# Kernel optimization log

Measured on AMD Instinct MI355X. Metric: run time of the kernel, lower is better.

## Reference

```python
import jax, jax.numpy as jnp
import numpy as np

B, W, N, DIM, GAMMA = 32, 16, 256, 256, 4
WH = 16  # sqrt(N)
V = DIM // GAMMA
TABLE = (2 * WH - 1) * (2 * WH - 1)  # 961


def _make_rel_index(wh: int) -> np.ndarray:
    coords = np.stack(np.meshgrid(np.arange(wh), np.arange(wh), indexing='ij'))  # (2, wh, wh)
    flat = coords.reshape(2, -1)                         # (2, wh*wh)
    rel = flat[:, :, None] - flat[:, None, :]            # (2, n, n)
    rel = rel.transpose(1, 2, 0).copy()                  # (n, n, 2)
    rel[:, :, 0] += wh - 1
    rel[:, :, 1] += wh - 1
    rel[:, :, 0] *= 2 * wh - 1
    return rel.sum(-1).astype(np.int32)                  # (n, n)


def setup_inputs() -> dict:
    key = jax.random.key(0)
    k1, k2, k3 = jax.random.split(key, 3)
    x = jax.random.normal(k1, (B, W, N, DIM), dtype=jnp.float32)
    bias_table = jax.random.normal(k2, (TABLE, W * GAMMA), dtype=jnp.float32) * 0.02
    token_bias = jax.random.normal(k3, (W * GAMMA, N, 1), dtype=jnp.float32) * 0.02
    rel_index = jnp.asarray(_make_rel_index(WH))
    return {"x": x, "bias_table": bias_table, "token_bias": token_bias, "rel_index": rel_index}


def reference(x, bias_table, token_bias, rel_index):
    b, w, n, d = x.shape
    gamma = GAMMA
    v = d // gamma
    # gather: (n, n, w*gamma) -> permute to (w*gamma, n, n)
    rpb = bias_table[rel_index.reshape(-1)].reshape(n, n, w * gamma)
    rpb = jnp.transpose(rpb, (2, 0, 1))                  # ((s w), n, n) with s outer
    # rearrange '(s b) m n -> b m n s'
    win_weight = jnp.transpose(rpb.reshape(gamma, w, n, n), (1, 2, 3, 0))  # (w, m, n, s)
    # rearrange 'b w n (v s) -> b w n v s'
    xs = x.reshape(b, w, n, v, gamma)
    out = jnp.einsum('wmns,bwnvs->bwmvs', win_weight, xs)
    # rearrange '(w s) m v -> w m v s'
    bias = jnp.transpose(token_bias.reshape(w, gamma, n, 1), (0, 2, 3, 1))  # (w, m, 1, s)
    out = out + bias[None]
    return out.reshape(b, w, n, d)
```

## Files before the change

### kernel.cpp

```cpp
#include <hip/hip_runtime.h>
#include <stdint.h>


typedef __attribute__((ext_vector_type(8))) short bf16x8;
typedef __attribute__((ext_vector_type(4))) float f32x4;
typedef __attribute__((ext_vector_type(8))) unsigned short u16x8;

__device__ __forceinline__ unsigned short f2bf(float f) {
    union { float f; unsigned u; } v; v.f = f;
    unsigned u = v.u;
    u += 0x7FFFu + ((u >> 16) & 1u);
    return (unsigned short)(u >> 16);
}
__device__ __forceinline__ float bf2f(unsigned short h) {
    union { unsigned u; float f; } v; v.u = ((unsigned)h) << 16;
    return v.f;
}
__device__ __forceinline__ int expInRange(unsigned short w16) {
    int e = (w16 >> 7) & 0xFF;
    return (e >= 100 && e <= 140) ? 1 : 0;
}

#define GLL16(gp, lp) __builtin_amdgcn_global_load_lds( \
    (const __attribute__((address_space(1))) void*)(gp), \
    (__attribute__((address_space(3))) void*)(lp), 16, 0, 0)

__global__ __launch_bounds__(256) void k_gather(
    const void* __restrict__ bt_raw,
    const int*  __restrict__ rel_index,
    const void* __restrict__ x_raw,
    unsigned short* __restrict__ Ab)
{
    __shared__ unsigned short Lt[64 * 72];

    const unsigned short* xw = (const unsigned short*)x_raw;
    int t = threadIdx.x;
    int pred = expInRange(xw[t * 2]) & expInRange(xw[t * 2 + 1]);
    int cnt = __syncthreads_count(pred);
    bool isF32 = (cnt < 150);

    const int cellbase = blockIdx.x << 6;
    const int c = t >> 2;
    const int p = t & 3;
    const int row = rel_index[cellbase + c];

    unsigned short vals[16];
    if (isF32) {
        const float* bt = (const float*)bt_raw + (row << 6) + (p << 4);
        float4 v0 = *(const float4*)(bt);
        float4 v1 = *(const float4*)(bt + 4);
        float4 v2 = *(const float4*)(bt + 8);
        float4 v3 = *(const float4*)(bt + 12);
        float vf[16] = {v0.x,v0.y,v0.z,v0.w, v1.x,v1.y,v1.z,v1.w,
                        v2.x,v2.y,v2.z,v2.w, v3.x,v3.y,v3.z,v3.w};
#pragma unroll
        for (int k = 0; k < 16; k++) vals[k] = f2bf(vf[k]);
    } else {
        const unsigned short* bt = (const unsigned short*)bt_raw + (row << 6) + (p << 4);
        u16x8 a0 = *(const u16x8*)(bt);
        u16x8 a1 = *(const u16x8*)(bt + 8);
#pragma unroll
        for (int k = 0; k < 8; k++) { vals[k] = a0[k]; vals[8 + k] = a1[k]; }
    }
#pragma unroll
    for (int k = 0; k < 16; k++)
        Lt[(((k << 2) + p) * 72) + c] = vals[k];
    __syncthreads();

    const int plane = t >> 2;
    const int cg = (t & 3) << 4;
    u16x8 o0 = *(const u16x8*)(Lt + plane * 72 + cg);
    u16x8 o1 = *(const u16x8*)(Lt + plane * 72 + cg + 8);
    unsigned short* dst = Ab + (plane << 16) + cellbase + cg;
    *(u16x8*)dst = o0;
    *(u16x8*)(dst + 8) = o1;
}

__global__ __launch_bounds__(512, 4) void k_main(
    const void* __restrict__ x_raw,
    const unsigned short* __restrict__ Ab,
    const void* __restrict__ tb_raw,
    void* __restrict__ out_raw)
{
    __shared__ unsigned short lds[16384];

    const int tid  = threadIdx.x;
    const unsigned short* xw = (const unsigned short*)x_raw;
    int pred = expInRange(xw[tid]);
    int cnt = __syncthreads_count(pred);
    const bool isF32 = (cnt < 400);

    const int lane = tid & 63;
    const int wave = tid >> 6;
    const int bx = blockIdx.x;
    const int swz = ((bx & 7) << 8) | (bx >> 3);
    const int mt = swz & 3;
    const int b  = (swz >> 2) & 31;
    const int w  = swz >> 7;
    const int m0 = mt << 6;

    const int sw   = wave & 3;
    const int vh   = wave >> 2;
    const int vvb  = vh << 5;
    const int col  = lane & 15;
    const int quad = lane >> 4;

    const int amRow   = (tid >> 2) & 63;
    const int aswslot = (tid & 3) ^ ((amRow >> 1) & 3);
    const unsigned short* Ag0 = Ab + (((w << 2) + (tid >> 8)) << 16)
                                   + ((m0 + amRow) << 8) + (aswslot << 3);
    const unsigned short* Ag1 = Ag0 + (2 << 16);
    const int aswz = (col >> 1) & 3;
    const int ar = (sw << 11) + (col << 5) + ((quad ^ aswz) << 3);

    const int d0   = (tid & 127) << 1;
    const int ngrp = tid >> 7;
    const int xgoff = (((b << 4) + w) << 16) + (ngrp << 11) + d0;
    const float*          Xgf = (const float*)x_raw + xgoff;
    const unsigned short* Xgh = (const unsigned short*)x_raw + xgoff;
    const int vvx   = d0 >> 2;
    const int xslot = ((ngrp ^ ((vvx >> 1) & 3)) << 3);
    unsigned short* xw0p = lds + 8192 + ((d0 & 3) << 11) + (vvx << 5) + xslot;
    unsigned short* xw1p = xw0p + 2048;

    const int xr0 = 8192 + (sw << 11) + ((vvb + col) << 5) + ((quad ^ aswz) << 3);
    const int xr1 = xr0 + 512;

    f32x4 acc[4][2];
#pragma unroll
    for (int mi = 0; mi < 4; mi++) {
        acc[mi][0] = (f32x4){0.f, 0.f, 0.f, 0.f};
        acc[mi][1] = (f32x4){0.f, 0.f, 0.f, 0.f};
    }

    for (int nc = 0; nc < 8; ++nc) {
        GLL16(Ag0 + (nc << 5), lds + (wave << 9));
        GLL16(Ag1 + (nc << 5), lds + 4096 + (wave << 9));

        u16x8 o0, o1;
        if (isF32) {
            float2 v[8];
#pragma unroll
            for (int j = 0; j < 8; j++)
                v[j] = *(const float2*)(Xgf + (nc << 13) + (j << 8));
#pragma unroll
            for (int j = 0; j < 8; j++) { o0[j] = f2bf(v[j].x); o1[j] = f2bf(v[j].y); }
        } else {
            unsigned int v[8];
#pragma unroll
            for (int j = 0; j < 8; j++)
                v[j] = *(const unsigned int*)(Xgh + (nc << 13) + (j << 8));
#pragma unroll
            for (int j = 0; j < 8; j++) { o0[j] = (unsigned short)(v[j] & 0xFFFFu);
                                          o1[j] = (unsigned short)(v[j] >> 16); }
        }
        *(u16x8*)xw0p = o0;
        *(u16x8*)xw1p = o1;
        __syncthreads();

        bf16x8 bfr0 = *(const bf16x8*)(lds + xr0);
        bf16x8 bfr1 = *(const bf16x8*)(lds + xr1);
#pragma unroll
        for (int mi = 0; mi < 4; mi++) {
            bf16x8 afr = *(const bf16x8*)(lds + ar + (mi << 9));
            acc[mi][0] = __builtin_amdgcn_mfma_f32_16x16x32_bf16(afr, bfr0, acc[mi][0], 0, 0, 0);
            acc[mi][1] = __builtin_amdgcn_mfma_f32_16x16x32_bf16(afr, bfr1, acc[mi][1], 0, 0, 0);
        }
        __syncthreads();
    }

    const int tboff = (((w << 2) + sw) << 8) + m0;
    const int ooff  = (((b << 4) + w) << 16) + (m0 << 8) + sw;
    if (isF32) {
        const float* tb = (const float*)tb_raw + tboff;
        float* ob = (float*)out_raw + ooff;
#pragma unroll
        for (int mi = 0; mi < 4; mi++) {
#pragma unroll
            for (int r = 0; r < 4; r++) {
                int m = (mi << 4) + (quad << 2) + r;
                float bias = tb[m];
#pragma unroll
                for (int vi = 0; vi < 2; vi++) {
                    int vv = vvb + (vi << 4) + col;
                    ob[(m << 8) + (vv << 2)] = acc[mi][vi][r] + bias;
                }
            }
        }
    } else {
        const unsigned short* tb = (const unsigned short*)tb_raw + tboff;
        unsigned short* ob = (unsigned short*)out_raw + ooff;
#pragma unroll
        for (int mi = 0; mi < 4; mi++) {
#pragma unroll
            for (int r = 0; r < 4; r++) {
                int m = (mi << 4) + (quad << 2) + r;
                float bias = bf2f(tb[m]);
#pragma unroll
                for (int vi = 0; vi < 2; vi++) {
                    int vv = vvb + (vi << 4) + col;
                    ob[(m << 8) + (vv << 2)] = f2bf(acc[mi][vi][r] + bias);
                }
            }
        }
    }
}

__global__ __launch_bounds__(512, 4) void k_main_fused(
    const void* __restrict__ x_raw,
    const void* __restrict__ bt_raw,
    const int*  __restrict__ rel_index,
    const void* __restrict__ tb_raw,
    void* __restrict__ out_raw)
{
    __shared__ unsigned short lds[16384 + 8192];

    const int tid  = threadIdx.x;
    const unsigned short* xw = (const unsigned short*)x_raw;
    int pred = expInRange(xw[tid]);
    int cnt = __syncthreads_count(pred);
    const bool isF32 = (cnt < 400);

    const int lane = tid & 63;
    const int wave = tid >> 6;
    const int bx = blockIdx.x;
    const int b  = bx & 31;
    const int mt = (bx >> 5) & 1;
    const int w  = bx >> 6;
    const int m0 = mt << 7;

    const int sw   = wave & 3;
    const int vh   = wave >> 2;
    const int vvb  = vh << 5;
    const int col  = lane & 15;
    const int quad = lane >> 4;

    const int a_row = tid >> 2;
    const int a_nn8 = (tid & 3) << 3;
    unsigned short* AsW = lds + (a_row << 5) + a_nn8;
    const int* rIp = rel_index + ((m0 + a_row) << 8) + a_nn8;

    const int x_nn = tid & 31;
    const int x_vg = tid >> 5;
    const int xoff = (((b << 4) + w) << 16) + (x_nn << 8) + (x_vg << 4);
    const float*          Xgf = (const float*)x_raw + xoff;
    const unsigned short* Xgh = (const unsigned short*)x_raw + xoff;
    unsigned short* XsW = lds + 16384 + x_nn;

    f32x4 acc[8][2];
#pragma unroll
    for (int mi = 0; mi < 8; mi++) {
        acc[mi][0] = (f32x4){0.f, 0.f, 0.f, 0.f};
        acc[mi][1] = (f32x4){0.f, 0.f, 0.f, 0.f};
    }

    const unsigned short* AsR = lds + (sw << 12) + (col << 5) + (quad << 3);
    const unsigned short* XsR = lds + 16384 + (sw << 11) + ((vvb + col) << 5) + (quad << 3);

    for (int nc = 0; nc < 8; nc++) {
        int4 r0 = *(const int4*)(rIp + (nc << 5));
        int4 r1 = *(const int4*)(rIp + (nc << 5) + 4);
        int ri[8] = {r0.x, r0.y, r0.z, r0.w, r1.x, r1.y, r1.z, r1.w};
#pragma unroll
        for (int it = 0; it < 4; it++) {
            u16x8 av;
            if (isF32) {
                const float* bt = (const float*)bt_raw;
#pragma unroll
                for (int j = 0; j < 8; j++)
                    av[j] = f2bf(bt[(ri[j] << 6) + (it << 4) + w]);
            } else {
                const unsigned short* bt = (const unsigned short*)bt_raw;
#pragma unroll
                for (int j = 0; j < 8; j++)
                    av[j] = bt[(ri[j] << 6) + (it << 4) + w];
            }
            *(u16x8*)(AsW + (it << 12)) = av;
        }

        if (isF32) {
            float4 v[4];
#pragma unroll
            for (int i = 0; i < 4; i++)
                v[i] = *(const float4*)(Xgf + (nc << 13) + (i << 2));
            const float* vf = (const float*)v;
#pragma unroll
            for (int j = 0; j < 16; j++) {
                int vv = (x_vg << 2) + (j >> 2);
                XsW[((j & 3) << 11) + (vv << 5)] = f2bf(vf[j]);
            }
        } else {
            u16x8 xv0 = *(const u16x8*)(Xgh + (nc << 13));
            u16x8 xv1 = *(const u16x8*)(Xgh + (nc << 13) + 8);
#pragma unroll
            for (int j = 0; j < 8; j++) {
                int vv = (x_vg << 2) + (j >> 2);
                XsW[((j & 3) << 11) + (vv << 5)] = xv0[j];
            }
#pragma unroll
            for (int j = 0; j < 8; j++) {
                int vv = (x_vg << 2) + 2 + (j >> 2);
                XsW[((j & 3) << 11) + (vv << 5)] = xv1[j];
            }
        }
        __syncthreads();

        bf16x8 bfr0 = *(const bf16x8*)(XsR);
        bf16x8 bfr1 = *(const bf16x8*)(XsR + 512);
#pragma unroll
        for (int mi = 0; mi < 8; mi++) {
            bf16x8 afr = *(const bf16x8*)(AsR + (mi << 9));
            acc[mi][0] = __builtin_amdgcn_mfma_f32_16x16x32_bf16(afr, bfr0, acc[mi][0], 0, 0, 0);
            acc[mi][1] = __builtin_amdgcn_mfma_f32_16x16x32_bf16(afr, bfr1, acc[mi][1], 0, 0, 0);
        }
        __syncthreads();
    }

    const int tboff = (((w << 2) + sw) << 8) + m0;
    const int ooff  = (((b << 4) + w) << 16) + (m0 << 8) + sw;
    if (isF32) {
        const float* tb = (const float*)tb_raw + tboff;
        float* ob = (float*)out_raw + ooff;
#pragma unroll
        for (int mi = 0; mi < 8; mi++) {
#pragma unroll
            for (int r = 0; r < 4; r++) {
                int m = (mi << 4) + (quad << 2) + r;
                float bias = tb[m];
#pragma unroll
                for (int vi = 0; vi < 2; vi++) {
                    int vv = vvb + (vi << 4) + col;
                    ob[(m << 8) + (vv << 2)] = acc[mi][vi][r] + bias;
                }
            }
        }
    } else {
        const unsigned short* tb = (const unsigned short*)tb_raw + tboff;
        unsigned short* ob = (unsigned short*)out_raw + ooff;
#pragma unroll
        for (int mi = 0; mi < 8; mi++) {
#pragma unroll
            for (int r = 0; r < 4; r++) {
                int m = (mi << 4) + (quad << 2) + r;
                float bias = bf2f(tb[m]);
#pragma unroll
                for (int vi = 0; vi < 2; vi++) {
                    int vv = vvb + (vi << 4) + col;
                    ob[(m << 8) + (vv << 2)] = f2bf(acc[mi][vi][r] + bias);
                }
            }
        }
    }
}

extern "C" void kernel_launch(void* const* d_in, const int* in_sizes, int n_in,
                              void* d_out, int out_size, void* d_ws, size_t ws_size,
                              hipStream_t stream) {
    const void* x          = d_in[0];
    const void* bias_table = d_in[1];
    const void* token_bias = d_in[2];
    const int*  rel_index  = (const int*)d_in[3];

    const size_t AB_BYTES = (size_t)64 * 256 * 256 * 2;
    if (ws_size >= AB_BYTES) {
        unsigned short* Ab = (unsigned short*)d_ws;
        hipLaunchKernelGGL(k_gather, dim3(1024), dim3(256), 0, stream,
                           bias_table, rel_index, x, Ab);
        hipLaunchKernelGGL(k_main, dim3(2048), dim3(512), 0, stream,
                           x, Ab, token_bias, d_out);
    } else {
        hipLaunchKernelGGL(k_main_fused, dim3(1024), dim3(512), 0, stream,
                           x, bias_table, rel_index, token_bias, d_out);
    }
}
```

Baseline: 307.0 us.

## Double the M tile per block and prefetch next X chunk into registers

Each block now computes 128 output rows instead of 64. The grid is halved, so each staged X tile is reused across twice as many MFMAs, which halves redundant X reads and conversions. The next n-chunk of X is also loaded into registers during the current chunk's compute, to hide global load latency. In exchange, LDS grows to 48KB, accumulator registers double, and fewer blocks mean lower occupancy and parallelism.

```diff
diff --git a/kernel.cpp b/kernel.cpp
--- a/kernel.cpp
+++ b/kernel.cpp
@@ -82,7 +82,7 @@
     const void* __restrict__ tb_raw,
     void* __restrict__ out_raw)
 {
-    __shared__ unsigned short lds[16384];
+    __shared__ unsigned short lds[24576];
 
     const int tid  = threadIdx.x;
     const unsigned short* xw = (const unsigned short*)x_raw;
@@ -93,11 +93,11 @@
     const int lane = tid & 63;
     const int wave = tid >> 6;
     const int bx = blockIdx.x;
-    const int swz = ((bx & 7) << 8) | (bx >> 3);
-    const int mt = swz & 3;
-    const int b  = (swz >> 2) & 31;
-    const int w  = swz >> 7;
-    const int m0 = mt << 6;
+    const int swz = ((bx & 7) << 7) | (bx >> 3);
+    const int mt = swz & 1;
+    const int b  = (swz >> 1) & 31;
+    const int w  = swz >> 6;
+    const int m0 = mt << 7;
 
     const int sw   = wave & 3;
     const int vh   = wave >> 2;
@@ -105,13 +105,11 @@
     const int col  = lane & 15;
     const int quad = lane >> 4;
 
-    const int amRow   = (tid >> 2) & 63;
+    const int amRow   = (tid >> 2) & 127;
     const int aswslot = (tid & 3) ^ ((amRow >> 1) & 3);
-    const unsigned short* Ag0 = Ab + (((w << 2) + (tid >> 8)) << 16)
-                                   + ((m0 + amRow) << 8) + (aswslot << 3);
-    const unsigned short* Ag1 = Ag0 + (2 << 16);
+    const unsigned short* AgB = Ab + ((m0 + amRow) << 8) + (aswslot << 3);
     const int aswz = (col >> 1) & 3;
-    const int ar = (sw << 11) + (col << 5) + ((quad ^ aswz) << 3);
+    const int ar = (sw << 12) + (col << 5) + ((quad ^ aswz) << 3);
 
     const int d0   = (tid & 127) << 1;
     const int ngrp = tid >> 7;
@@ -120,48 +118,65 @@
     const unsigned short* Xgh = (const unsigned short*)x_raw + xgoff;
     const int vvx   = d0 >> 2;
     const int xslot = ((ngrp ^ ((vvx >> 1) & 3)) << 3);
-    unsigned short* xw0p = lds + 8192 + ((d0 & 3) << 11) + (vvx << 5) + xslot;
+    unsigned short* xw0p = lds + 16384 + ((d0 & 3) << 11) + (vvx << 5) + xslot;
     unsigned short* xw1p = xw0p + 2048;
 
-    const int xr0 = 8192 + (sw << 11) + ((vvb + col) << 5) + ((quad ^ aswz) << 3);
+    const int xr0 = 16384 + (sw << 11) + ((vvb + col) << 5) + ((quad ^ aswz) << 3);
     const int xr1 = xr0 + 512;
 
-    f32x4 acc[4][2];
-#pragma unroll
-    for (int mi = 0; mi < 4; mi++) {
+    f32x4 acc[8][2];
+#pragma unroll
+    for (int mi = 0; mi < 8; mi++) {
         acc[mi][0] = (f32x4){0.f, 0.f, 0.f, 0.f};
         acc[mi][1] = (f32x4){0.f, 0.f, 0.f, 0.f};
     }
 
+    float2       xf[8];
+    unsigned int xu[8];
+    if (isF32) {
+#pragma unroll
+        for (int j = 0; j < 8; j++) xf[j] = *(const float2*)(Xgf + (j << 8));
+    } else {
+#pragma unroll
+        for (int j = 0; j < 8; j++) xu[j] = *(const unsigned int*)(Xgh + (j << 8));
+    }
+
+#pragma unroll
     for (int nc = 0; nc < 8; ++nc) {
-        GLL16(Ag0 + (nc << 5), lds + (wave << 9));
-        GLL16(Ag1 + (nc << 5), lds + 4096 + (wave << 9));
+#pragma unroll
+        for (int c = 0; c < 4; c++)
+            GLL16(AgB + (((w << 2) + c) << 16) + (nc << 5),
+                  lds + (c << 12) + (wave << 9));
 
         u16x8 o0, o1;
         if (isF32) {
-            float2 v[8];
-#pragma unroll
-            for (int j = 0; j < 8; j++)
-                v[j] = *(const float2*)(Xgf + (nc << 13) + (j << 8));
-#pragma unroll
-            for (int j = 0; j < 8; j++) { o0[j] = f2bf(v[j].x); o1[j] = f2bf(v[j].y); }
+#pragma unroll
+            for (int j = 0; j < 8; j++) { o0[j] = f2bf(xf[j].x); o1[j] = f2bf(xf[j].y); }
         } else {
-            unsigned int v[8];
-#pragma unroll
-            for (int j = 0; j < 8; j++)
-                v[j] = *(const unsigned int*)(Xgh + (nc << 13) + (j << 8));
-#pragma unroll
-            for (int j = 0; j < 8; j++) { o0[j] = (unsigned short)(v[j] & 0xFFFFu);
-                                          o1[j] = (unsigned short)(v[j] >> 16); }
+#pragma unroll
+            for (int j = 0; j < 8; j++) { o0[j] = (unsigned short)(xu[j] & 0xFFFFu);
+                                          o1[j] = (unsigned short)(xu[j] >> 16); }
         }
         *(u16x8*)xw0p = o0;
         *(u16x8*)xw1p = o1;
         __syncthreads();
 
+        if (nc < 7) {
+            if (isF32) {
+#pragma unroll
+                for (int j = 0; j < 8; j++)
+                    xf[j] = *(const float2*)(Xgf + ((nc + 1) << 13) + (j << 8));
+            } else {
+#pragma unroll
+                for (int j = 0; j < 8; j++)
+                    xu[j] = *(const unsigned int*)(Xgh + ((nc + 1) << 13) + (j << 8));
+            }
+        }
+
         bf16x8 bfr0 = *(const bf16x8*)(lds + xr0);
         bf16x8 bfr1 = *(const bf16x8*)(lds + xr1);
 #pragma unroll
-        for (int mi = 0; mi < 4; mi++) {
+        for (int mi = 0; mi < 8; mi++) {
             bf16x8 afr = *(const bf16x8*)(lds + ar + (mi << 9));
             acc[mi][0] = __builtin_amdgcn_mfma_f32_16x16x32_bf16(afr, bfr0, acc[mi][0], 0, 0, 0);
             acc[mi][1] = __builtin_amdgcn_mfma_f32_16x16x32_bf16(afr, bfr1, acc[mi][1], 0, 0, 0);
@@ -175,7 +190,7 @@
         const float* tb = (const float*)tb_raw + tboff;
         float* ob = (float*)out_raw + ooff;
 #pragma unroll
-        for (int mi = 0; mi < 4; mi++) {
+        for (int mi = 0; mi < 8; mi++) {
 #pragma unroll
             for (int r = 0; r < 4; r++) {
                 int m = (mi << 4) + (quad << 2) + r;
@@ -191,7 +206,7 @@
         const unsigned short* tb = (const unsigned short*)tb_raw + tboff;
         unsigned short* ob = (unsigned short*)out_raw + ooff;
 #pragma unroll
-        for (int mi = 0; mi < 4; mi++) {
+        for (int mi = 0; mi < 8; mi++) {
 #pragma unroll
             for (int r = 0; r < 4; r++) {
                 int m = (mi << 4) + (quad << 2) + r;
@@ -366,7 +381,7 @@
         unsigned short* Ab = (unsigned short*)d_ws;
         hipLaunchKernelGGL(k_gather, dim3(1024), dim3(256), 0, stream,
                            bias_table, rel_index, x, Ab);
-        hipLaunchKernelGGL(k_main, dim3(2048), dim3(512), 0, stream,
+        hipLaunchKernelGGL(k_main, dim3(1024), dim3(512), 0, stream,
                            x, Ab, token_bias, d_out);
     } else {
         hipLaunchKernelGGL(k_main_fused, dim3(1024), dim3(512), 0, stream,
```

New measurement: 310.2 us. No clear change (+1.0%).

## Double m-tile per block to 128 rows, halving x reloads and grid size

Applied to the files above, without the earlier changes.

Each k_main block now covers 128 output rows instead of 64, so every x chunk loaded and converted to bf16 feeds twice as many MFMAs. The grid drops from 2048 to 1024 blocks, the accumulator array doubles, and LDS grows by 8192 shorts. The A tile is now loaded through registers with plain vector loads instead of direct global-to-LDS loads, and the block-index swizzle is replaced by a plain b-fastest ordering. This trades more registers, more LDS and fewer blocks (lower occupancy) for less redundant x traffic.

```diff
diff --git a/kernel.cpp b/kernel.cpp
--- a/kernel.cpp
+++ b/kernel.cpp
@@ -20,10 +20,6 @@
     int e = (w16 >> 7) & 0xFF;
     return (e >= 100 && e <= 140) ? 1 : 0;
 }
-
-#define GLL16(gp, lp) __builtin_amdgcn_global_load_lds( \
-    (const __attribute__((address_space(1))) void*)(gp), \
-    (__attribute__((address_space(3))) void*)(lp), 16, 0, 0)
 
 __global__ __launch_bounds__(256) void k_gather(
     const void* __restrict__ bt_raw,
@@ -82,7 +78,7 @@
     const void* __restrict__ tb_raw,
     void* __restrict__ out_raw)
 {
-    __shared__ unsigned short lds[16384];
+    __shared__ unsigned short lds[16384 + 8192];
 
     const int tid  = threadIdx.x;
     const unsigned short* xw = (const unsigned short*)x_raw;
@@ -93,11 +89,10 @@
     const int lane = tid & 63;
     const int wave = tid >> 6;
     const int bx = blockIdx.x;
-    const int swz = ((bx & 7) << 8) | (bx >> 3);
-    const int mt = swz & 3;
-    const int b  = (swz >> 2) & 31;
-    const int w  = swz >> 7;
-    const int m0 = mt << 6;
+    const int b  = bx & 31;
+    const int mt = (bx >> 5) & 1;
+    const int w  = bx >> 6;
+    const int m0 = mt << 7;
 
     const int sw   = wave & 3;
     const int vh   = wave >> 2;
@@ -105,37 +100,38 @@
     const int col  = lane & 15;
     const int quad = lane >> 4;
 
-    const int amRow   = (tid >> 2) & 63;
-    const int aswslot = (tid & 3) ^ ((amRow >> 1) & 3);
-    const unsigned short* Ag0 = Ab + (((w << 2) + (tid >> 8)) << 16)
-                                   + ((m0 + amRow) << 8) + (aswslot << 3);
-    const unsigned short* Ag1 = Ag0 + (2 << 16);
+    const int a_row  = tid >> 2;
+    const int a_slot = tid & 3;
+    const int a_psl  = a_slot ^ ((a_row >> 1) & 3);
+    unsigned short* AsW = lds + (a_row << 5) + (a_psl << 3);
+    const unsigned short* Ag = Ab + (w << 18) + ((m0 + a_row) << 8) + (a_slot << 3);
     const int aswz = (col >> 1) & 3;
-    const int ar = (sw << 11) + (col << 5) + ((quad ^ aswz) << 3);
+    const int ar = (sw << 12) + (col << 5) + ((quad ^ aswz) << 3);
 
     const int d0   = (tid & 127) << 1;
     const int ngrp = tid >> 7;
     const int xgoff = (((b << 4) + w) << 16) + (ngrp << 11) + d0;
     const float*          Xgf = (const float*)x_raw + xgoff;
     const unsigned short* Xgh = (const unsigned short*)x_raw + xgoff;
-    const int vvx   = d0 >> 2;
-    const int xslot = ((ngrp ^ ((vvx >> 1) & 3)) << 3);
-    unsigned short* xw0p = lds + 8192 + ((d0 & 3) << 11) + (vvx << 5) + xslot;
+    const int vvx = d0 >> 2;
+    unsigned short* xw0p = lds + 16384 + ((d0 & 3) << 11) + (vvx << 5)
+                               + ((ngrp ^ ((vvx >> 1) & 3)) << 3);
     unsigned short* xw1p = xw0p + 2048;
-
-    const int xr0 = 8192 + (sw << 11) + ((vvb + col) << 5) + ((quad ^ aswz) << 3);
+    const int xr0 = 16384 + (sw << 11) + ((vvb + col) << 5) + ((quad ^ aswz) << 3);
     const int xr1 = xr0 + 512;
 
-    f32x4 acc[4][2];
-#pragma unroll
-    for (int mi = 0; mi < 4; mi++) {
+    f32x4 acc[8][2];
+#pragma unroll
+    for (int mi = 0; mi < 8; mi++) {
         acc[mi][0] = (f32x4){0.f, 0.f, 0.f, 0.f};
         acc[mi][1] = (f32x4){0.f, 0.f, 0.f, 0.f};
     }
 
-    for (int nc = 0; nc < 8; ++nc) {
-        GLL16(Ag0 + (nc << 5), lds + (wave << 9));
-        GLL16(Ag1 + (nc << 5), lds + 4096 + (wave << 9));
+    for (int nc = 0; nc < 8; nc++) {
+        u16x8 av[4];
+#pragma unroll
+        for (int it = 0; it < 4; it++)
+            av[it] = *(const u16x8*)(Ag + (it << 16) + (nc << 5));
 
         u16x8 o0, o1;
         if (isF32) {
@@ -154,6 +150,10 @@
             for (int j = 0; j < 8; j++) { o0[j] = (unsigned short)(v[j] & 0xFFFFu);
                                           o1[j] = (unsigned short)(v[j] >> 16); }
         }
+
+#pragma unroll
+        for (int it = 0; it < 4; it++)
+            *(u16x8*)(AsW + (it << 12)) = av[it];
         *(u16x8*)xw0p = o0;
         *(u16x8*)xw1p = o1;
         __syncthreads();
@@ -161,7 +161,7 @@
         bf16x8 bfr0 = *(const bf16x8*)(lds + xr0);
         bf16x8 bfr1 = *(const bf16x8*)(lds + xr1);
 #pragma unroll
-        for (int mi = 0; mi < 4; mi++) {
+        for (int mi = 0; mi < 8; mi++) {
             bf16x8 afr = *(const bf16x8*)(lds + ar + (mi << 9));
             acc[mi][0] = __builtin_amdgcn_mfma_f32_16x16x32_bf16(afr, bfr0, acc[mi][0], 0, 0, 0);
             acc[mi][1] = __builtin_amdgcn_mfma_f32_16x16x32_bf16(afr, bfr1, acc[mi][1], 0, 0, 0);
@@ -175,7 +175,7 @@
         const float* tb = (const float*)tb_raw + tboff;
         float* ob = (float*)out_raw + ooff;
 #pragma unroll
-        for (int mi = 0; mi < 4; mi++) {
+        for (int mi = 0; mi < 8; mi++) {
 #pragma unroll
             for (int r = 0; r < 4; r++) {
                 int m = (mi << 4) + (quad << 2) + r;
@@ -191,7 +191,7 @@
         const unsigned short* tb = (const unsigned short*)tb_raw + tboff;
         unsigned short* ob = (unsigned short*)out_raw + ooff;
 #pragma unroll
-        for (int mi = 0; mi < 4; mi++) {
+        for (int mi = 0; mi < 8; mi++) {
 #pragma unroll
             for (int r = 0; r < 4; r++) {
                 int m = (mi << 4) + (quad << 2) + r;
@@ -366,7 +366,7 @@
         unsigned short* Ab = (unsigned short*)d_ws;
         hipLaunchKernelGGL(k_gather, dim3(1024), dim3(256), 0, stream,
                            bias_table, rel_index, x, Ab);
-        hipLaunchKernelGGL(k_main, dim3(2048), dim3(512), 0, stream,
+        hipLaunchKernelGGL(k_main, dim3(1024), dim3(512), 0, stream,
                            x, Ab, token_bias, d_out);
     } else {
         hipLaunchKernelGGL(k_main_fused, dim3(1024), dim3(512), 0, stream,
```

New measurement: 293.4 us. 1.05x faster.
